# Kernel tuning notes

Measured on AMD Instinct MI355X. Metric: run time of the kernel, lower is better.

Reference implementation:

```python
import jax, jax.numpy as jnp
import numpy as np

EPS = 1e-5

def conv2d(x, w, b=None, pad=1):
    y = jax.lax.conv_general_dilated(x, w, (1, 1), [(pad, pad), (pad, pad)],
                                     dimension_numbers=('NCHW', 'OIHW', 'NCHW'))
    if b is not None:
        y = y + b[None, :, None, None]
    return y

def batchnorm(x, g, b):
    m = x.mean((0, 2, 3), keepdims=True)
    v = x.var((0, 2, 3), keepdims=True)
    return g[None, :, None, None] * (x - m) * jax.lax.rsqrt(v + EPS) + b[None, :, None, None]

def local_conv(x, w12):
    # x: [B,Ci,H,W]; w12: [B,Ci*9,H,W] -> per-pixel depthwise 3x3 conv
    B, Ci, H, W = x.shape
    xp = jnp.pad(x, ((0, 0), (0, 0), (1, 1), (1, 1)))
    patches = jnp.stack([xp[:, :, dh:dh + H, dw:dw + W]
                         for dh in range(3) for dw in range(3)], axis=2)  # [B,Ci,9,H,W]
    return (patches * w12.reshape(B, Ci, 9, H, W)).sum(axis=2)

def setup_inputs() -> dict:
    key = jax.random.key(0)
    ks = jax.random.split(key, 20)
    B, Ci, Cw, H, W = 4, 64, 64, 128, 128
    s = 0.05
    return {
        'input': jax.random.normal(ks[0], (B, Ci, H, W), jnp.float32),
        'weight': jax.random.normal(ks[1], (B, Cw, H, W), jnp.float32),
        'w_conv11': jax.random.normal(ks[2], (Ci, Ci + Cw, 3, 3), jnp.float32) * s,
        'b_conv11': jnp.zeros((Ci,), jnp.float32),
        'w_conv12': jax.random.normal(ks[3], (Ci * 9, Ci, 3, 3), jnp.float32) * s,
        'b_conv12': jnp.zeros((Ci * 9,), jnp.float32),
        'w_conv21': jax.random.normal(ks[4], (Ci, Ci + Cw, 3, 3), jnp.float32) * s,
        'b_conv21': jnp.zeros((Ci,), jnp.float32),
        'w_conv22': jax.random.normal(ks[5], (Ci * Ci, Ci, 1, 1), jnp.float32) * s,
        'b_conv22': jnp.zeros((Ci * Ci,), jnp.float32),
        'local_bn_g': jnp.ones((Ci,), jnp.float32),
        'local_bn_b': jnp.zeros((Ci,), jnp.float32),
        'br_g': jnp.ones((Ci,), jnp.float32),
        'br_b': jnp.zeros((Ci,), jnp.float32),
        'w_conv3': jax.random.normal(ks[6], (Ci, Ci, 3, 3), jnp.float32) * s,
        'conv3_bn_g': jnp.ones((Ci,), jnp.float32),
        'conv3_bn_b': jnp.zeros((Ci,), jnp.float32),
    }

def reference(input, weight, w_conv11, b_conv11, w_conv12, b_conv12,
              w_conv21, b_conv21, w_conv22, b_conv22,
              local_bn_g, local_bn_b, br_g, br_b,
              w_conv3, conv3_bn_g, conv3_bn_b):
    B, Ci, H, W = input.shape
    cat = jnp.concatenate([input, weight], axis=1)
    w11 = jax.nn.relu(conv2d(cat, w_conv11, b_conv11))
    w12 = conv2d(w11, w_conv12, b_conv12)                      # [B,Ci*9,H,W]
    w21 = jax.nn.relu(conv2d(cat, w_conv21, b_conv21))
    pooled = w21.mean((2, 3), keepdims=True)                   # [B,Ci,1,1]
    w22 = conv2d(pooled, w_conv22, b_conv22, pad=0).reshape(B, Ci, Ci)
    out1 = jax.nn.relu(batchnorm(local_conv(input, w12), local_bn_g, local_bn_b))
    out2 = jnp.einsum('bij,bjn->bin', w22, out1.reshape(B, Ci, H * W)).reshape(B, Ci, H, W)
    out3 = jax.nn.relu(batchnorm(out2, br_g, br_b))
    out4 = jax.nn.relu(batchnorm(conv2d(out3, w_conv3, None), conv3_bn_g, conv3_bn_b))
    return out4
```

## Files before the change

### kernel.cpp

```cpp
#include <hip/hip_runtime.h>

#define EPSV 1e-5f
#define HP 130
#define HW 16384

typedef unsigned int u32;
typedef unsigned short bfu;
typedef __bf16 bf16x8 __attribute__((ext_vector_type(8)));
typedef float  f32x4  __attribute__((ext_vector_type(4)));

__device__ __forceinline__ bfu f2bf(float f){
  u32 u = __builtin_bit_cast(u32, f);
  return (bfu)((u + 0x7FFFu + ((u >> 16) & 1u)) >> 16);
}
__device__ __forceinline__ float bf2f(bfu h){
  return __builtin_bit_cast(float, ((u32)h) << 16);
}
__device__ __forceinline__ f32x4 mfma16(bf16x8 a, bf16x8 b, f32x4 c){
  return __builtin_amdgcn_mfma_f32_16x16x32_bf16(a, b, c, 0, 0, 0);
}
__device__ __forceinline__ bf16x8 ldsfrag(const bfu* p){
  return __builtin_bit_cast(bf16x8, *(const uint4*)p);
}
__device__ __forceinline__ void gload_lds16(const uint4* g, uint4* l){
  __builtin_amdgcn_global_load_lds(
      (const __attribute__((address_space(1))) unsigned int*)g,
      (__attribute__((address_space(3))) unsigned int*)l, 16, 0, 0);
}


__global__ void k_zero_border(bfu* catT, bfu* w11T, bfu* out3T){
  int i = blockIdx.x*256 + threadIdx.x;
  if (i >= 4*516) return;
  int b = i/516, r = i - b*516;
  int hp, wpp;
  if (r < 130){ hp = 0; wpp = r; }
  else if (r < 260){ hp = 129; wpp = r - 130; }
  else { int r2 = r - 260; hp = 1 + (r2 >> 1); wpp = (r2 & 1)*129; }
  int pix = (b*HP + hp)*HP + wpp;
  uint4 z = {0,0,0,0};
  uint4* c4 = (uint4*)catT  + (size_t)pix*16;
  uint4* w4 = (uint4*)w11T  + (size_t)pix*8;
  uint4* o4 = (uint4*)out3T + (size_t)pix*8;
  #pragma unroll
  for (int k = 0; k < 16; ++k) c4[k] = z;
  #pragma unroll
  for (int k = 0; k < 8; ++k){ w4[k] = z; o4[k] = z; }
}

__global__ void k_prep_w(const float* __restrict__ w11w, const float* __restrict__ w21w,
                         const float* __restrict__ w12w, const float* __restrict__ w3w,
                         bfu* A11, bfu* A12, bfu* A3){
  const int total = 147456 + 331776 + 36864;
  for (int i = blockIdx.x*256 + threadIdx.x; i < total; i += gridDim.x*256){
    float v; bfu* dst;
    if (i < 147456){
      int tap = i >> 14, och = (i >> 7) & 127, cin = i & 127;
      v = (och < 64) ? w11w[(och*128 + cin)*9 + tap] : w21w[((och-64)*128 + cin)*9 + tap];
      dst = A11 + i;
    } else if (i < 147456 + 331776){
      int i2 = i - 147456;
      int g = i2 >> 12, t = g/9, tap2 = g%9;
      int c = (i2 >> 6) & 63, j = i2 & 63;
      v = w12w[((c*9 + t)*64 + j)*9 + tap2];
      dst = A12 + i2;
    } else {
      int i3 = i - (147456 + 331776);
      int tap2 = i3 >> 12, oc = (i3 >> 6) & 63, j = i3 & 63;
      v = w3w[(oc*64 + j)*9 + tap2];
      dst = A3 + i3;
    }
    *dst = f2bf(v);
  }
}

__global__ void k_prep_cat(const float* __restrict__ inp, const float* __restrict__ wgt, bfu* catT){
  __shared__ bfu lds[128*136];
  int b = blockIdx.y, h = blockIdx.x;
  int t = threadIdx.x;
  int w = t & 127, c0 = t >> 7;
  #pragma unroll 1
  for (int c = c0; c < 128; c += 2){
    const float* src = (c < 64) ? inp + ((b*64 + c)*128 + h)*128
                                : wgt + ((b*64 + (c-64))*128 + h)*128;
    lds[w*136 + c] = f2bf(src[w]);
  }
  __syncthreads();
  uint4* dst = (uint4*)catT;
  #pragma unroll
  for (int k = 0; k < 8; ++k){
    int idx = k*256 + t;
    int pix = idx >> 4, sub = idx & 15;
    uint4 v = *(const uint4*)&lds[pix*136 + sub*8];
    dst[(((b*HP + h+1)*HP) + (pix+1))*16 + sub] = v;
  }
}

__global__ __launch_bounds__(256) void k1_conv(
    const bfu* __restrict__ catT, const bfu* __restrict__ A11,
    const float* __restrict__ b11, const float* __restrict__ b21,
    bfu* __restrict__ w11T, float* __restrict__ poolP){
  __shared__ bfu lds[24480];
  int tid = threadIdx.x;
  int b = blockIdx.y, tile = blockIdx.x;
  int h0 = (tile >> 3)*8, w0 = (tile & 7)*16;

  const uint4* catT4 = (const uint4*)catT;
  for (int s = tid; s < 180*17; s += 256){
    int cell = s/17, sub = s%17;
    if (sub < 16){
      int th = cell/18, tw = cell%18;
      uint4 v = catT4[(((b*HP + h0+th)*HP) + (w0+tw))*16 + sub];
      *(uint4*)&lds[cell*136 + sub*8] = v;
    }
  }
  __syncthreads();

  int wid = tid >> 6, l = tid & 63, lg = l >> 4, pc = l & 15;
  int wm = wid >> 1, wn = wid & 1;
  f32x4 acc[4][4];
  #pragma unroll
  for (int i = 0; i < 4; ++i)
    #pragma unroll
    for (int j = 0; j < 4; ++j) acc[i][j] = f32x4{0.f,0.f,0.f,0.f};

  const uint4* A4 = (const uint4*)A11;
  #pragma unroll 3
  for (int tap = 0; tap < 9; ++tap){
    int kh = tap/3, kw = tap%3;
    #pragma unroll
    for (int jc = 0; jc < 4; ++jc){
      bf16x8 a[4], bb[4];
      #pragma unroll
      for (int fm = 0; fm < 4; ++fm){
        int row = wm*64 + fm*16 + pc;
        a[fm] = __builtin_bit_cast(bf16x8, A4[(tap*128 + row)*16 + jc*4 + lg]);
      }
      #pragma unroll
      for (int fn = 0; fn < 4; ++fn){
        int cell = (wn*4 + fn + kh)*18 + (pc + kw);
        bb[fn] = ldsfrag(&lds[cell*136 + jc*32 + lg*8]);
      }
      #pragma unroll
      for (int fm = 0; fm < 4; ++fm)
        #pragma unroll
        for (int fn = 0; fn < 4; ++fn)
          acc[fm][fn] = mfma16(a[fm], bb[fn], acc[fm][fn]);
    }
  }
  __syncthreads();

  if (wm == 0){
    #pragma unroll
    for (int fm = 0; fm < 4; ++fm)
      #pragma unroll
      for (int r = 0; r < 4; ++r){
        int och = fm*16 + lg*4 + r;
        float bias = b11[och];
        #pragma unroll
        for (int fn = 0; fn < 4; ++fn){
          float v = acc[fm][fn][r] + bias;
          v = v > 0.f ? v : 0.f;
          int px = wn*64 + fn*16 + pc;
          lds[px*72 + och] = f2bf(v);
        }
      }
  } else {
    float* statsF = (float*)&lds[20000];
    #pragma unroll
    for (int fm = 0; fm < 4; ++fm)
      #pragma unroll
      for (int r = 0; r < 4; ++r){
        int cw = fm*16 + lg*4 + r;
        float bias = b21[cw];
        float s = 0.f;
        #pragma unroll
        for (int fn = 0; fn < 4; ++fn){
          float v = acc[fm][fn][r] + bias;
          s += (v > 0.f ? v : 0.f);
        }
        s += __shfl_xor(s,1); s += __shfl_xor(s,2); s += __shfl_xor(s,4); s += __shfl_xor(s,8);
        if (pc == 0) statsF[wn*64 + cw] = s;
      }
  }
  __syncthreads();

  if (wid < 2){
    int px = tid;
    int h = h0 + (px >> 4), w = w0 + (px & 15);
    uint4* dst = (uint4*)w11T + (((b*HP + h+1)*HP) + (w+1))*8;
    const uint4* srcT = (const uint4*)&lds[px*72];
    #pragma unroll
    for (int k = 0; k < 8; ++k) dst[k] = srcT[k];
  }
  if (tid < 64){
    float* statsF = (float*)&lds[20000];
    poolP[(b*128 + tile)*64 + tid] = statsF[tid] + statsF[64 + tid];
  }
}

__global__ void k2a_pool(const float* __restrict__ poolP, float* pooled){
  int t = threadIdx.x;
  int b = t >> 6, c = t & 63;
  float s = 0.f;
  for (int tile = 0; tile < 128; ++tile) s += poolP[(b*128 + tile)*64 + c];
  pooled[t] = s * (1.f/16384.f);
}

__global__ void k2b_w22(const float* __restrict__ pooled, const float* __restrict__ W22,
                        const float* __restrict__ b22, bfu* __restrict__ w22bf){
  __shared__ float pl[64];
  int b = blockIdx.x >> 4, og = blockIdx.x & 15;
  if (threadIdx.x < 64) pl[threadIdx.x] = pooled[b*64 + threadIdx.x];
  __syncthreads();
  int o = og*256 + threadIdx.x;
  float acc = b22[o];
  #pragma unroll 4
  for (int c = 0; c < 64; ++c) acc += pl[c]*W22[o*64 + c];
  w22bf[b*4096 + o] = f2bf(acc);
}

__global__ __launch_bounds__(256) void k3_fused(
    const bfu* __restrict__ w11T, const bfu* __restrict__ catT,
    const bfu* __restrict__ A12, const float* __restrict__ b12,
    float* __restrict__ out1, float* __restrict__ st1){
  __shared__ bfu ldsW[180*64];
  __shared__ bfu ldsA[2*1536*8];
  __shared__ float b12f[576];
  __shared__ float wp[512];
  int tid = threadIdx.x;
  int b = blockIdx.y, tile = blockIdx.x;
  int h0 = (tile >> 3)*8, w0 = (tile & 7)*16;

  int wid = tid >> 6, l = tid & 63, lg = l >> 4, pc = l & 15;
  int w2 = wid*2;

  const uint4* A4 = (const uint4*)A12;
  uint4* ldsA4 = (uint4*)ldsA;
  int srcA = ((tid >> 7)*16 + (tid & 15))*8 + ((tid >> 6) & 1)*4 + ((tid >> 4) & 3);
  uint4* dstBase = ldsA4 + wid*64;

  {
    const uint4* sb = A4 + srcA;
    #pragma unroll
    for (int q = 0; q < 6; ++q)
      gload_lds16(sb + (q>>1)*512 + ((q&1)<<8), dstBase + (q>>1)*512 + ((q&1)<<8));
  }

  const uint4* w11T4 = (const uint4*)w11T;
  for (int s = tid; s < 180*8; s += 256){
    int cell = s >> 3, sub = s & 7;
    int th = cell/18, tw = cell - th*18;
    uint4 v = w11T4[(((b*HP + h0+th)*HP) + (w0+tw))*8 + sub];
    *(uint4*)&ldsW[cell*64 + ((sub*8) ^ ((cell&7)<<3))] = v;
  }
  for (int i = tid; i < 576; i += 256) b12f[i] = b12[i];
  __syncthreads();

  f32x4 oacc[4][2];
  #pragma unroll
  for (int i = 0; i < 4; ++i){ oacc[i][0] = f32x4{0.f,0.f,0.f,0.f}; oacc[i][1] = f32x4{0.f,0.f,0.f,0.f}; }
  f32x4 y[4][2];
  int cur = 0;

  #pragma unroll 1
  for (int cc = 0; cc < 27; ++cc){
    int tt = cc/3, m3 = cc - tt*3;
    if (cc < 26){
      const uint4* sb = A4 + (size_t)((cc+1)*3)*512 + srcA;
      uint4* db = dstBase + (cur^1)*1536;
      #pragma unroll
      for (int q = 0; q < 6; ++q)
        gload_lds16(sb + (q>>1)*512 + ((q&1)<<8), db + (q>>1)*512 + ((q&1)<<8));
    }
    if (m3 == 0){
      #pragma unroll
      for (int i = 0; i < 4; ++i){ y[i][0] = f32x4{0.f,0.f,0.f,0.f}; y[i][1] = f32x4{0.f,0.f,0.f,0.f}; }
    }
    #pragma unroll
    for (int t3 = 0; t3 < 3; ++t3){
      #pragma unroll
      for (int jc = 0; jc < 2; ++jc){
        bf16x8 a[4], bbf[2];
        #pragma unroll
        for (int fm = 0; fm < 4; ++fm)
          a[fm] = __builtin_bit_cast(bf16x8, ldsA4[cur*1536 + t3*512 + (fm*2 + jc)*64 + l]);
        #pragma unroll
        for (int fn = 0; fn < 2; ++fn){
          int cell = (w2 + fn + m3)*18 + (pc + t3);
          bbf[fn] = ldsfrag(&ldsW[cell*64 + ((jc*32 + lg*8) ^ ((cell&7)<<3))]);
        }
        #pragma unroll
        for (int fm = 0; fm < 4; ++fm)
          #pragma unroll
          for (int fn = 0; fn < 2; ++fn)
            y[fm][fn] = mfma16(a[fm], bbf[fn], y[fm][fn]);
      }
    }
    __syncthreads();
    if (m3 == 2){
      int dh = tt/3, dw = tt - dh*3;
      #pragma unroll
      for (int fn = 0; fn < 2; ++fn){
        const bfu* base = catT + ((size_t)((b*HP + h0 + w2 + fn + dh)*HP) + (w0 + pc + dw))*128 + lg*4;
        #pragma unroll
        for (int fm = 0; fm < 4; ++fm){
          ushort4 iv = *(const ushort4*)(base + fm*16);
          float i0 = bf2f(iv.x), i1 = bf2f(iv.y), i2 = bf2f(iv.z), i3 = bf2f(iv.w);
          int c = fm*16 + lg*4;
          oacc[fm][fn][0] += i0 * (y[fm][fn][0] + b12f[(c+0)*9 + tt]);
          oacc[fm][fn][1] += i1 * (y[fm][fn][1] + b12f[(c+1)*9 + tt]);
          oacc[fm][fn][2] += i2 * (y[fm][fn][2] + b12f[(c+2)*9 + tt]);
          oacc[fm][fn][3] += i3 * (y[fm][fn][3] + b12f[(c+3)*9 + tt]);
        }
      }
    }
    cur ^= 1;
  }

  #pragma unroll
  for (int fm = 0; fm < 4; ++fm)
    #pragma unroll
    for (int r = 0; r < 4; ++r){
      int c = fm*16 + lg*4 + r;
      float s = 0.f, ss = 0.f;
      #pragma unroll
      for (int fn = 0; fn < 2; ++fn){
        float v = oacc[fm][fn][r];
        out1[((b*64 + c)*128 + h0 + w2 + fn)*128 + (w0 + pc)] = v;
        s += v; ss += v*v;
      }
      s += __shfl_xor(s,1); s += __shfl_xor(s,2); s += __shfl_xor(s,4); s += __shfl_xor(s,8);
      ss += __shfl_xor(ss,1); ss += __shfl_xor(ss,2); ss += __shfl_xor(ss,4); ss += __shfl_xor(ss,8);
      if (pc == 0){ wp[(wid*64 + c)*2] = s; wp[(wid*64 + c)*2 + 1] = ss; }
    }
  __syncthreads();
  if (tid < 64){
    float s = 0.f, ss = 0.f;
    #pragma unroll
    for (int w = 0; w < 4; ++w){ s += wp[(w*64 + tid)*2]; ss += wp[(w*64 + tid)*2 + 1]; }
    int blin = b*128 + tile;
    st1[(blin*64 + tid)*2] = s; st1[(blin*64 + tid)*2 + 1] = ss;
  }
}

__global__ void k_bnstat(const float* __restrict__ st, int nblk, float n,
                         const float* __restrict__ g, const float* __restrict__ bb, float* bn){
  __shared__ float red[512];
  int tid = threadIdx.x;
  int c = tid & 63, kk = tid >> 6;
  float s = 0.f, ss = 0.f;
  for (int k = kk; k < nblk; k += 4){
    float2 v = *(const float2*)&st[(k*64 + c)*2];
    s += v.x; ss += v.y;
  }
  red[tid*2] = s; red[tid*2 + 1] = ss;
  __syncthreads();
  if (tid < 64){
    #pragma unroll
    for (int q = 1; q < 4; ++q){ s += red[(q*64 + tid)*2]; ss += red[(q*64 + tid)*2 + 1]; }
    float mean = s/n, var = ss/n - mean*mean;
    float a = g[tid]*rsqrtf(var + EPSV);
    bn[tid*2] = a; bn[tid*2 + 1] = bb[tid] - mean*a;
  }
}

__global__ __launch_bounds__(256) void k4_einsum(
    const float* __restrict__ out1, const bfu* __restrict__ w22bf,
    const float* __restrict__ bn1, float* __restrict__ out2, float* __restrict__ st2){
  __shared__ bfu ldsX[256*72];
  __shared__ float a1[64], be1[64];
  __shared__ float wp[512];
  int tid = threadIdx.x;
  int b = blockIdx.y, chunk = blockIdx.x;
  if (tid < 64){ a1[tid] = bn1[tid*2]; be1[tid] = bn1[tid*2 + 1]; }
  __syncthreads();
  int p0 = chunk*256;

  {
    int px = tid;
    const float* src = out1 + (size_t)(b*64)*HW + p0 + px;
    #pragma unroll 1
    for (int j0 = 0; j0 < 64; j0 += 4){
      float x0 = src[(j0+0)*HW]; x0 = a1[j0+0]*x0 + be1[j0+0]; x0 = x0 > 0.f ? x0 : 0.f;
      float x1 = src[(j0+1)*HW]; x1 = a1[j0+1]*x1 + be1[j0+1]; x1 = x1 > 0.f ? x1 : 0.f;
      float x2 = src[(j0+2)*HW]; x2 = a1[j0+2]*x2 + be1[j0+2]; x2 = x2 > 0.f ? x2 : 0.f;
      float x3 = src[(j0+3)*HW]; x3 = a1[j0+3]*x3 + be1[j0+3]; x3 = x3 > 0.f ? x3 : 0.f;
      ushort4 pk; pk.x = f2bf(x0); pk.y = f2bf(x1); pk.z = f2bf(x2); pk.w = f2bf(x3);
      *(ushort4*)&ldsX[px*72 + j0] = pk;
    }
  }
  __syncthreads();

  int wid = tid >> 6, l = tid & 63, lg = l >> 4, pc = l & 15;
  const uint4* W4 = (const uint4*)w22bf;
  f32x4 acc[4][4];
  #pragma unroll
  for (int i = 0; i < 4; ++i)
    #pragma unroll
    for (int j = 0; j < 4; ++j) acc[i][j] = f32x4{0.f,0.f,0.f,0.f};

  #pragma unroll
  for (int jc = 0; jc < 2; ++jc){
    bf16x8 a[4], bb[4];
    #pragma unroll
    for (int fm = 0; fm < 4; ++fm)
      a[fm] = __builtin_bit_cast(bf16x8, W4[b*512 + (fm*16 + pc)*8 + jc*4 + lg]);
    #pragma unroll
    for (int fn = 0; fn < 4; ++fn)
      bb[fn] = ldsfrag(&ldsX[(wid*64 + fn*16 + pc)*72 + jc*32 + lg*8]);
    #pragma unroll
    for (int fm = 0; fm < 4; ++fm)
      #pragma unroll
      for (int fn = 0; fn < 4; ++fn)
        acc[fm][fn] = mfma16(a[fm], bb[fn], acc[fm][fn]);
  }

  #pragma unroll
  for (int fm = 0; fm < 4; ++fm)
    #pragma unroll
    for (int r = 0; r < 4; ++r){
      int i = fm*16 + lg*4 + r;
      float s = 0.f, ss = 0.f;
      #pragma unroll
      for (int fn = 0; fn < 4; ++fn){
        int px = wid*64 + fn*16 + pc;
        float v = acc[fm][fn][r];
        out2[(b*64 + i)*HW + p0 + px] = v;
        s += v; ss += v*v;
      }
      s += __shfl_xor(s,1); s += __shfl_xor(s,2); s += __shfl_xor(s,4); s += __shfl_xor(s,8);
      ss += __shfl_xor(ss,1); ss += __shfl_xor(ss,2); ss += __shfl_xor(ss,4); ss += __shfl_xor(ss,8);
      if (pc == 0){ wp[(wid*64 + i)*2] = s; wp[(wid*64 + i)*2 + 1] = ss; }
    }
  __syncthreads();
  if (tid < 64){
    float s = 0.f, ss = 0.f;
    #pragma unroll
    for (int w = 0; w < 4; ++w){ s += wp[(w*64 + tid)*2]; ss += wp[(w*64 + tid)*2 + 1]; }
    int blin = b*64 + chunk;
    st2[(blin*64 + tid)*2] = s; st2[(blin*64 + tid)*2 + 1] = ss;
  }
}

__global__ void k4c_out3(const float* __restrict__ out2, const float* __restrict__ bn2, bfu* out3T){
  __shared__ bfu lds[128*72];
  int b = blockIdx.y, h = blockIdx.x;
  int t = threadIdx.x;
  int px = t & 127, ch = (t >> 7)*32;
  #pragma unroll 1
  for (int cc = 0; cc < 32; cc += 4){
    int c = ch + cc;
    float x0 = out2[((b*64 + c+0) << 14) + (h << 7) + px];
    float x1 = out2[((b*64 + c+1) << 14) + (h << 7) + px];
    float x2 = out2[((b*64 + c+2) << 14) + (h << 7) + px];
    float x3 = out2[((b*64 + c+3) << 14) + (h << 7) + px];
    x0 = bn2[(c+0)*2]*x0 + bn2[(c+0)*2+1]; x0 = x0 > 0.f ? x0 : 0.f;
    x1 = bn2[(c+1)*2]*x1 + bn2[(c+1)*2+1]; x1 = x1 > 0.f ? x1 : 0.f;
    x2 = bn2[(c+2)*2]*x2 + bn2[(c+2)*2+1]; x2 = x2 > 0.f ? x2 : 0.f;
    x3 = bn2[(c+3)*2]*x3 + bn2[(c+3)*2+1]; x3 = x3 > 0.f ? x3 : 0.f;
    ushort4 pk; pk.x = f2bf(x0); pk.y = f2bf(x1); pk.z = f2bf(x2); pk.w = f2bf(x3);
    *(ushort4*)&lds[px*72 + c] = pk;
  }
  __syncthreads();
  uint4* dst = (uint4*)out3T;
  #pragma unroll
  for (int k = 0; k < 4; ++k){
    int idx = k*256 + t;
    int pix = idx >> 3, sub = idx & 7;
    uint4 v = *(const uint4*)&lds[pix*72 + sub*8];
    dst[((size_t)(b*HP + h+1)*HP + (pix+1))*8 + sub] = v;
  }
}

__global__ __launch_bounds__(256) void k5_conv3(
    const bfu* __restrict__ out3T, const bfu* __restrict__ A3,
    float* __restrict__ outc, float* __restrict__ st3){
  __shared__ bfu lds[180*72];
  __shared__ float wp[512];
  int tid = threadIdx.x;
  int b = blockIdx.y, tile = blockIdx.x;
  int h0 = (tile >> 3)*8, w0 = (tile & 7)*16;
  const uint4* src4 = (const uint4*)out3T;
  for (int s = tid; s < 180*8; s += 256){
    int cell = s >> 3, sub = s & 7;
    int th = cell/18, tw = cell - th*18;
    *(uint4*)&lds[cell*72 + sub*8] = src4[(((b*HP + h0+th)*HP) + (w0+tw))*8 + sub];
  }
  __syncthreads();

  int wid = tid >> 6, l = tid & 63, lg = l >> 4, pc = l & 15;
  f32x4 acc[4][2];
  #pragma unroll
  for (int i = 0; i < 4; ++i){ acc[i][0] = f32x4{0.f,0.f,0.f,0.f}; acc[i][1] = f32x4{0.f,0.f,0.f,0.f}; }
  const uint4* A4 = (const uint4*)A3;
  #pragma unroll 3
  for (int tap2 = 0; tap2 < 9; ++tap2){
    int kh = tap2/3, kw = tap2 - kh*3;
    #pragma unroll
    for (int jc = 0; jc < 2; ++jc){
      bf16x8 a[4], bb[2];
      #pragma unroll
      for (int fm = 0; fm < 4; ++fm)
        a[fm] = __builtin_bit_cast(bf16x8, A4[tap2*512 + (fm*16 + pc)*8 + jc*4 + lg]);
      #pragma unroll
      for (int fn = 0; fn < 2; ++fn){
        int cell = (wid*2 + fn + kh)*18 + (pc + kw);
        bb[fn] = ldsfrag(&lds[cell*72 + jc*32 + lg*8]);
      }
      #pragma unroll
      for (int fm = 0; fm < 4; ++fm)
        #pragma unroll
        for (int fn = 0; fn < 2; ++fn)
          acc[fm][fn] = mfma16(a[fm], bb[fn], acc[fm][fn]);
    }
  }
  #pragma unroll
  for (int fm = 0; fm < 4; ++fm)
    #pragma unroll
    for (int r = 0; r < 4; ++r){
      int c = fm*16 + lg*4 + r;
      float s = 0.f, ss = 0.f;
      #pragma unroll
      for (int fn = 0; fn < 2; ++fn){
        int pr = wid*2 + fn;
        float v = acc[fm][fn][r];
        outc[((b*64 + c)*128 + h0 + pr)*128 + (w0 + pc)] = v;
        s += v; ss += v*v;
      }
      s += __shfl_xor(s,1); s += __shfl_xor(s,2); s += __shfl_xor(s,4); s += __shfl_xor(s,8);
      ss += __shfl_xor(ss,1); ss += __shfl_xor(ss,2); ss += __shfl_xor(ss,4); ss += __shfl_xor(ss,8);
      if (pc == 0){ wp[(wid*64 + c)*2] = s; wp[(wid*64 + c)*2 + 1] = ss; }
    }
  __syncthreads();
  if (tid < 64){
    float s = 0.f, ss = 0.f;
    #pragma unroll
    for (int w = 0; w < 4; ++w){ s += wp[(w*64 + tid)*2]; ss += wp[(w*64 + tid)*2 + 1]; }
    int blin = b*128 + tile;
    st3[(blin*64 + tid)*2] = s; st3[(blin*64 + tid)*2 + 1] = ss;
  }
}

__global__ void k6_final(float4* __restrict__ out, const float* __restrict__ bn3){
  const int total4 = 4*64*HW/4;
  for (int i = blockIdx.x*256 + threadIdx.x; i < total4; i += gridDim.x*256){
    int c = (i >> 12) & 63;
    float a = bn3[c*2], be = bn3[c*2 + 1];
    float4 x = out[i];
    x.x = a*x.x + be; x.x = x.x > 0.f ? x.x : 0.f;
    x.y = a*x.y + be; x.y = x.y > 0.f ? x.y : 0.f;
    x.z = a*x.z + be; x.z = x.z > 0.f ? x.z : 0.f;
    x.w = a*x.w + be; x.w = x.w > 0.f ? x.w : 0.f;
    out[i] = x;
  }
}

extern "C" void kernel_launch(void* const* d_in, const int* in_sizes, int n_in,
                              void* d_out, int out_size, void* d_ws, size_t ws_size,
                              hipStream_t stream){
  const float* inp  = (const float*)d_in[0];
  const float* wgt  = (const float*)d_in[1];
  const float* w11w = (const float*)d_in[2];
  const float* b11  = (const float*)d_in[3];
  const float* w12w = (const float*)d_in[4];
  const float* b12  = (const float*)d_in[5];
  const float* w21w = (const float*)d_in[6];
  const float* b21  = (const float*)d_in[7];
  const float* W22  = (const float*)d_in[8];
  const float* b22  = (const float*)d_in[9];
  const float* lg   = (const float*)d_in[10];
  const float* lb   = (const float*)d_in[11];
  const float* brg  = (const float*)d_in[12];
  const float* brb  = (const float*)d_in[13];
  const float* w3w  = (const float*)d_in[14];
  const float* c3g  = (const float*)d_in[15];
  const float* c3b  = (const float*)d_in[16];

  if (ws_size < 53200000) return;

  char* ws = (char*)d_ws;
  bfu*   catT  = (bfu*)(ws);
  bfu*   w11T  = (bfu*)(ws + 17305600);
  bfu*   out3T = (bfu*)(ws + 25958400);
  bfu*   A11   = (bfu*)(ws + 34611200);
  bfu*   A12   = (bfu*)(ws + 34906112);
  bfu*   A3    = (bfu*)(ws + 35569664);
  float* out1  = (float*)(ws + 35643392);
  float* poolP = (float*)(ws + 52420608);
  float* pooled= (float*)(ws + 52551680);
  bfu*   w22bf = (bfu*)(ws + 52552704);
  float* st13  = (float*)(ws + 52585472);
  float* bn1   = (float*)(ws + 52847616);
  float* st2   = (float*)(ws + 52848128);
  float* bn2   = (float*)(ws + 52979200);
  float* bn3   = (float*)(ws + 52979712);
  float* outF  = (float*)d_out;

  k_zero_border<<<dim3(9),  dim3(256), 0, stream>>>(catT, w11T, out3T);
  k_prep_w  <<<dim3(512),  dim3(256), 0, stream>>>(w11w, w21w, w12w, w3w, A11, A12, A3);
  k_prep_cat<<<dim3(128,4),dim3(256), 0, stream>>>(inp, wgt, catT);
  k1_conv   <<<dim3(128,4),dim3(256), 0, stream>>>(catT, A11, b11, b21, w11T, poolP);
  k2a_pool  <<<dim3(1),    dim3(256), 0, stream>>>(poolP, pooled);
  k2b_w22   <<<dim3(64),   dim3(256), 0, stream>>>(pooled, W22, b22, w22bf);
  k3_fused  <<<dim3(128,4),dim3(256), 0, stream>>>(w11T, catT, A12, b12, out1, st13);
  k_bnstat  <<<dim3(1),    dim3(256), 0, stream>>>(st13, 512, 65536.f, lg, lb, bn1);
  k4_einsum <<<dim3(64,4), dim3(256), 0, stream>>>(out1, w22bf, bn1, outF, st2);
  k_bnstat  <<<dim3(1),    dim3(256), 0, stream>>>(st2, 256, 65536.f, brg, brb, bn2);
  k4c_out3  <<<dim3(128,4),dim3(256), 0, stream>>>(outF, bn2, out3T);
  k5_conv3  <<<dim3(128,4),dim3(256), 0, stream>>>(out3T, A3, outF, st13);
  k_bnstat  <<<dim3(1),    dim3(256), 0, stream>>>(st13, 512, 65536.f, c3g, c3b, bn3);
  k6_final  <<<dim3(1024), dim3(256), 0, stream>>>((float4*)outF, bn3);
}
```

Baseline: 286.7 us.

## Stage conv11/21 weights through double-buffered LDS and swizzle the input tile

In the first conv kernel, weight fragments are now read from a double-buffered LDS area that is filled with asynchronous global-to-LDS loads one half-tap ahead, instead of being read from global memory inside the MFMA loop. The input tile in LDS drops its padded row stride in favour of an XOR swizzle to avoid bank conflicts. This is meant to hide the latency of the global weight loads and cut LDS conflicts. In exchange there is a barrier on each of 18 iterations, and LDS use rises, which may lower occupancy.

```diff
diff --git a/kernel.cpp b/kernel.cpp
--- a/kernel.cpp
+++ b/kernel.cpp
@@ -100,46 +100,69 @@
     const bfu* __restrict__ catT, const bfu* __restrict__ A11,
     const float* __restrict__ b11, const float* __restrict__ b21,
     bfu* __restrict__ w11T, float* __restrict__ poolP){
-  __shared__ bfu lds[24480];
+  __shared__ bfu ldsC[180*128];
+  __shared__ bfu ldsA[2*8192];
+  __shared__ float statsF[128];
   int tid = threadIdx.x;
   int b = blockIdx.y, tile = blockIdx.x;
   int h0 = (tile >> 3)*8, w0 = (tile & 7)*16;
 
-  const uint4* catT4 = (const uint4*)catT;
-  for (int s = tid; s < 180*17; s += 256){
-    int cell = s/17, sub = s%17;
-    if (sub < 16){
-      int th = cell/18, tw = cell%18;
-      uint4 v = catT4[(((b*HP + h0+th)*HP) + (w0+tw))*16 + sub];
-      *(uint4*)&lds[cell*136 + sub*8] = v;
-    }
-  }
-  __syncthreads();
-
   int wid = tid >> 6, l = tid & 63, lg = l >> 4, pc = l & 15;
   int wm = wid >> 1, wn = wid & 1;
+  int pcT = tid & 15, lgT = (tid >> 4) & 3;
+
+  const uint4* A4 = (const uint4*)A11;
+  uint4* ldsA4 = (uint4*)ldsA;
+
+  #pragma unroll
+  for (int k = 0; k < 4; ++k){
+    int q = k*4 + wid;
+    int row = (q >> 1)*16 + pcT;
+    gload_lds16(A4 + row*16 + (q&1)*4 + lgT, ldsA4 + k*256 + wid*64);
+  }
+
+  const uint4* catT4 = (const uint4*)catT;
+  for (int s = tid; s < 180*16; s += 256){
+    int cell = s >> 4, sub = s & 15;
+    int th = cell/18, tw = cell - th*18;
+    uint4 v = catT4[(((b*HP + h0+th)*HP) + (w0+tw))*16 + sub];
+    *(uint4*)&ldsC[cell*128 + ((sub*8) ^ ((cell&7)<<3))] = v;
+  }
+  __syncthreads();
+
   f32x4 acc[4][4];
   #pragma unroll
   for (int i = 0; i < 4; ++i)
     #pragma unroll
     for (int j = 0; j < 4; ++j) acc[i][j] = f32x4{0.f,0.f,0.f,0.f};
 
-  const uint4* A4 = (const uint4*)A11;
-  #pragma unroll 3
-  for (int tap = 0; tap < 9; ++tap){
-    int kh = tap/3, kw = tap%3;
-    #pragma unroll
-    for (int jc = 0; jc < 4; ++jc){
+  int cur = 0;
+  #pragma unroll 1
+  for (int cc = 0; cc < 18; ++cc){
+    int tap = cc >> 1, p = cc & 1;
+    if (cc < 17){
+      int cc1 = cc + 1, tap1 = cc1 >> 1, p1 = cc1 & 1;
+      #pragma unroll
+      for (int k = 0; k < 4; ++k){
+        int q = k*4 + wid;
+        int row = (q >> 1)*16 + pcT;
+        gload_lds16(A4 + tap1*2048 + row*16 + p1*8 + (q&1)*4 + lgT,
+                    ldsA4 + (cur^1)*1024 + k*256 + wid*64);
+      }
+    }
+    int kh = (tap >= 6) ? 2 : ((tap >= 3) ? 1 : 0);
+    int kw = tap - kh*3;
+    #pragma unroll
+    for (int jq = 0; jq < 2; ++jq){
+      int jc = p*2 + jq;
       bf16x8 a[4], bb[4];
       #pragma unroll
-      for (int fm = 0; fm < 4; ++fm){
-        int row = wm*64 + fm*16 + pc;
-        a[fm] = __builtin_bit_cast(bf16x8, A4[(tap*128 + row)*16 + jc*4 + lg]);
-      }
+      for (int fm = 0; fm < 4; ++fm)
+        a[fm] = __builtin_bit_cast(bf16x8, ldsA4[cur*1024 + ((wm*4 + fm)*2 + jq)*64 + l]);
       #pragma unroll
       for (int fn = 0; fn < 4; ++fn){
         int cell = (wn*4 + fn + kh)*18 + (pc + kw);
-        bb[fn] = ldsfrag(&lds[cell*136 + jc*32 + lg*8]);
+        bb[fn] = ldsfrag(&ldsC[cell*128 + ((jc*32 + lg*8) ^ ((cell&7)<<3))]);
       }
       #pragma unroll
       for (int fm = 0; fm < 4; ++fm)
@@ -147,8 +170,9 @@
         for (int fn = 0; fn < 4; ++fn)
           acc[fm][fn] = mfma16(a[fm], bb[fn], acc[fm][fn]);
     }
-  }
-  __syncthreads();
+    __syncthreads();
+    cur ^= 1;
+  }
 
   if (wm == 0){
     #pragma unroll
@@ -162,11 +186,10 @@
           float v = acc[fm][fn][r] + bias;
           v = v > 0.f ? v : 0.f;
           int px = wn*64 + fn*16 + pc;
-          lds[px*72 + och] = f2bf(v);
+          ldsC[px*72 + och] = f2bf(v);
         }
       }
   } else {
-    float* statsF = (float*)&lds[20000];
     #pragma unroll
     for (int fm = 0; fm < 4; ++fm)
       #pragma unroll
@@ -189,14 +212,12 @@
     int px = tid;
     int h = h0 + (px >> 4), w = w0 + (px & 15);
     uint4* dst = (uint4*)w11T + (((b*HP + h+1)*HP) + (w+1))*8;
-    const uint4* srcT = (const uint4*)&lds[px*72];
+    const uint4* srcT = (const uint4*)&ldsC[px*72];
     #pragma unroll
     for (int k = 0; k < 8; ++k) dst[k] = srcT[k];
   }
-  if (tid < 64){
-    float* statsF = (float*)&lds[20000];
+  if (tid < 64)
     poolP[(b*128 + tile)*64 + tid] = statsF[tid] + statsF[64 + tid];
-  }
 }
 
 __global__ void k2a_pool(const float* __restrict__ poolP, float* pooled){
```

Result: faster. 275.3 us (-4.0%).
